# Performance work log

Measured on AMD Instinct MI355X. Metric: run time of the kernel, lower is better.

The kernel has to match this reference:

```python
import jax, jax.numpy as jnp
import numpy as np

B, T = 32, 512
DA, DV = 1280, 768
D = DA + DV          # fused audio+video feature dim = 2048
DM = 256             # mamba d_model
L = 4                # n_layers
DI = 2 * DM          # d_inner (expand=2)
DS = 16              # d_state
DC = 4               # d_conv
R = DM // 16         # dt_rank = ceil(256/16)
H = 128              # attn-pool hidden
NC = 8               # emotion classes
EPS_TIN = 1e-5
EPS_LN = 1e-5


def _ln(x, g, b):
    mu = x.mean(-1, keepdims=True)
    v = ((x - mu) ** 2).mean(-1, keepdims=True)
    return (x - mu) / jnp.sqrt(v + EPS_LN) * g + b


def _mamba(u, in_w, cw, cb, xw, dtw, dtb, A_log, Dp, ow):
    # u: [B,T,DM] -> [B,T,DM]; Mamba(v1) selective scan, d_state=16, d_conv=4, expand=2
    xz = jnp.einsum('btd,ed->bte', u, in_w)            # [B,T,2*DI]
    x, z = xz[..., :DI], xz[..., DI:]
    xp = jnp.pad(x, ((0, 0), (DC - 1, 0), (0, 0)))     # causal depthwise conv1d
    xc = sum(xp[:, k:k + u.shape[1], :] * cw[:, k] for k in range(DC)) + cb
    x = jax.nn.silu(xc)
    dbc = jnp.einsum('btd,ed->bte', x, xw)             # [B,T,R+2*DS]
    dt = jax.nn.softplus(jnp.einsum('btr,dr->btd', dbc[..., :R], dtw) + dtb)
    Bm = dbc[..., R:R + DS]
    Cm = dbc[..., R + DS:]
    A = -jnp.exp(A_log)                                # [DI,DS]

    def step(h, inp):
        dt_t, B_t, C_t, x_t = inp                      # [B,DI],[B,DS],[B,DS],[B,DI]
        h = jnp.exp(dt_t[..., None] * A) * h + dt_t[..., None] * B_t[:, None, :] * x_t[..., None]
        return h, jnp.einsum('bds,bs->bd', h, C_t)

    h0 = jnp.zeros((u.shape[0], DI, DS), u.dtype)
    xs = (dt.swapaxes(0, 1), Bm.swapaxes(0, 1), Cm.swapaxes(0, 1), x.swapaxes(0, 1))
    _, ys = jax.lax.scan(step, h0, xs)
    y = ys.swapaxes(0, 1) + Dp * x
    y = y * jax.nn.silu(z)
    return jnp.einsum('bti,oi->bto', y, ow)


def _forward(x, tin_gamma, tin_beta, proj_w, proj_b, ln_g, ln_b, in_proj_w, conv_w, conv_b,
             x_proj_w, dt_proj_w, dt_proj_b, A_log, D_param, out_proj_w,
             out_ln_g, out_ln_b, res_scale, attn_w1, attn_b1, attn_w2, head_w, head_b, lengths):
    mask = jnp.arange(T)[None, :] < lengths[:, None]   # [B,T]
    m = mask[..., None].astype(x.dtype)
    # FusedTIN: masked temporal instance norm + affine
    denom = jnp.maximum(lengths, 1).astype(x.dtype)[:, None, None]
    mean = (x * m).sum(1, keepdims=True) / denom
    var = (((x - mean) ** 2) * m).sum(1, keepdims=True) / denom
    xn = (x - mean) / jnp.sqrt(var + EPS_TIN) * m
    xn = (xn * tin_gamma + tin_beta) * m
    # MambaStack: proj_in + prenorm residual mamba blocks (dropout = eval identity)
    h = jnp.einsum('btd,md->btm', xn, proj_w) + proj_b
    for l in range(L):
        y = _mamba(_ln(h, ln_g[l], ln_b[l]), in_proj_w[l], conv_w[l], conv_b[l],
                   x_proj_w[l], dt_proj_w[l], dt_proj_b[l], A_log[l], D_param[l], out_proj_w[l])
        h = h + res_scale * y
    h = _ln(h, out_ln_g, out_ln_b)
    # MaskedAttnPool
    s = jnp.einsum('bth,oh->bto', jnp.tanh(jnp.einsum('btd,hd->bth', h, attn_w1) + attn_b1), attn_w2)[..., 0]
    logits = jnp.where(mask, s, -jnp.inf)
    alpha = jnp.nan_to_num(jax.nn.softmax(logits, axis=1)) * mask
    alpha = alpha / jnp.clip(alpha.sum(1, keepdims=True), 1e-9)
    ctx = (alpha[..., None] * h).sum(1)
    # classifier head
    return jnp.einsum('bd,cd->bc', ctx, head_w) + head_b


def setup_inputs() -> dict:
    key = jax.random.key(0)
    ks = jax.random.split(key, 16)
    s = 0.05
    inp = {}
    inp['x'] = jax.random.normal(ks[0], (B, T, D), jnp.float32)
    inp['lengths'] = jax.random.randint(ks[1], (B,), T // 4, T + 1)
    inp['tin_gamma'] = jnp.ones((D,), jnp.float32)
    inp['tin_beta'] = jnp.zeros((D,), jnp.float32)
    inp['proj_w'] = jax.random.normal(ks[2], (DM, D), jnp.float32) * s
    inp['proj_b'] = jnp.zeros((DM,), jnp.float32)
    inp['ln_g'] = jnp.ones((L, DM), jnp.float32)
    inp['ln_b'] = jnp.zeros((L, DM), jnp.float32)
    inp['in_proj_w'] = jax.random.normal(ks[3], (L, 2 * DI, DM), jnp.float32) * s
    inp['conv_w'] = jax.random.normal(ks[4], (L, DI, DC), jnp.float32) * s
    inp['conv_b'] = jnp.zeros((L, DI), jnp.float32)
    inp['x_proj_w'] = jax.random.normal(ks[5], (L, R + 2 * DS, DI), jnp.float32) * s
    inp['dt_proj_w'] = jax.random.normal(ks[6], (L, DI, R), jnp.float32) * s
    inp['dt_proj_b'] = jnp.full((L, DI), -3.0, jnp.float32) + jax.random.normal(ks[7], (L, DI), jnp.float32) * 0.1
    inp['A_log'] = jnp.log(jnp.broadcast_to(jnp.arange(1, DS + 1, dtype=jnp.float32), (L, DI, DS)) + 0.0)
    inp['D_param'] = jnp.ones((L, DI), jnp.float32)
    inp['out_proj_w'] = jax.random.normal(ks[8], (L, DM, DI), jnp.float32) * s
    inp['out_ln_g'] = jnp.ones((DM,), jnp.float32)
    inp['out_ln_b'] = jnp.zeros((DM,), jnp.float32)
    inp['res_scale'] = jnp.asarray(0.1, jnp.float32)
    inp['attn_w1'] = jax.random.normal(ks[9], (H, DM), jnp.float32) * s
    inp['attn_b1'] = jnp.zeros((H,), jnp.float32)
    inp['attn_w2'] = jax.random.normal(ks[10], (1, H), jnp.float32) * s
    inp['head_w'] = jax.random.normal(ks[11], (NC, DM), jnp.float32) * s
    inp['head_b'] = jnp.zeros((NC,), jnp.float32)
    return inp


def reference(x, tin_gamma, tin_beta, proj_w, proj_b, ln_g, ln_b, in_proj_w, conv_w, conv_b,
              x_proj_w, dt_proj_w, dt_proj_b, A_log, D_param, out_proj_w,
              out_ln_g, out_ln_b, res_scale, attn_w1, attn_b1, attn_w2, head_w, head_b, lengths):
    return _forward(x, tin_gamma, tin_beta, proj_w, proj_b, ln_g, ln_b, in_proj_w, conv_w, conv_b,
                    x_proj_w, dt_proj_w, dt_proj_b, A_log, D_param, out_proj_w,
                    out_ln_g, out_ln_b, res_scale, attn_w1, attn_b1, attn_w2, head_w, head_b, lengths)
```

## Files before the change

### kernel.cpp

```cpp
#include <hip/hip_runtime.h>

#define NB 32
#define NT 512
#define ND 2048
#define NDM 256
#define NDI 512
#define NDS 16
#define NR 16
#define NH 128
#define NNC 8
#define NL 4
#define NM (NB*NT)

typedef __attribute__((ext_vector_type(8))) short short8;
typedef __attribute__((ext_vector_type(4))) float floatx4;

__device__ __forceinline__ unsigned short f2bf_rn(float f) {
    unsigned u = __builtin_bit_cast(unsigned, f);
    u += 0x7FFFu + ((u >> 16) & 1u);
    return (unsigned short)(u >> 16);
}
__device__ __forceinline__ void cvt8(const float* v, short8& h8, short8& l8) {
#pragma unroll
    for (int q = 0; q < 8; ++q) {
        unsigned short hb = f2bf_rn(v[q]);
        float hf = __builtin_bit_cast(float, (unsigned)hb << 16);
        h8[q] = (short)hb;
        l8[q] = (short)f2bf_rn(v[q] - hf);
    }
}

__global__ __launch_bounds__(256) void tin_stats_k(
    const float* __restrict__ x, const int* __restrict__ lengths,
    float* __restrict__ mean, float* __restrict__ rstd)
{
    __shared__ float rs_[4][64];
    __shared__ float rq_[4][64];
    const int b = blockIdx.x >> 5;
    const int d0 = (blockIdx.x & 31) << 6;
    const int dl = threadIdx.x & 63;
    const int strip = threadIdx.x >> 6;
    const int len = lengths[b];
    const int d = d0 + dl;
    float s = 0.f, q = 0.f;
    for (int t = strip; t < len; t += 4) {
        float v = x[((size_t)(b*NT + t))*ND + d];
        s += v; q += v*v;
    }
    rs_[strip][dl] = s; rq_[strip][dl] = q;
    __syncthreads();
    if (threadIdx.x < 64) {
        float S = rs_[0][dl]+rs_[1][dl]+rs_[2][dl]+rs_[3][dl];
        float Q = rq_[0][dl]+rq_[1][dl]+rq_[2][dl]+rq_[3][dl];
        float inv = 1.f / (float)(len < 1 ? 1 : len);
        float mu = S * inv;
        float var = Q * inv - mu*mu;
        mean[b*ND + d] = mu;
        rstd[b*ND + d] = rsqrtf(var + 1e-5f);
    }
}

#define SLN 264
__global__ __launch_bounds__(256) void tin_norm_k(
    const float* __restrict__ x, const int* __restrict__ lengths,
    const float* __restrict__ mean, const float* __restrict__ rstd,
    const float* __restrict__ g, const float* __restrict__ be,
    short* __restrict__ Oh, short* __restrict__ Ol)
{
    __shared__ float sT[16][SLN];
    const int tid = threadIdx.x;
    const int row = tid >> 4, c = tid & 15;
    const int m = blockIdx.x*16 + row;
    const int b = m >> 9, t = m & (NT-1);
    const int len = lengths[b];
    const int kg0 = blockIdx.y*256 + c*16;
    if (t >= len) {
#pragma unroll
        for (int i = 0; i < 16; ++i) sT[row][c*16 + i] = 0.f;
    } else {
#pragma unroll
        for (int qq = 0; qq < 4; ++qq) {
            const int kg = kg0 + qq*4;
            float4 v = *(const float4*)(x + (size_t)m*ND + kg);
            float4 mn = *(const float4*)(mean + b*ND + kg);
            float4 rr = *(const float4*)(rstd + b*ND + kg);
            float4 gg = *(const float4*)(g + kg);
            float4 bb = *(const float4*)(be + kg);
            sT[row][c*16+qq*4+0] = (v.x-mn.x)*rr.x*gg.x + bb.x;
            sT[row][c*16+qq*4+1] = (v.y-mn.y)*rr.y*gg.y + bb.y;
            sT[row][c*16+qq*4+2] = (v.z-mn.z)*rr.z*gg.z + bb.z;
            sT[row][c*16+qq*4+3] = (v.w-mn.w)*rr.w*gg.w + bb.w;
        }
    }
    __syncthreads();
#pragma unroll
    for (int q = 0; q < 2; ++q) {
        const int slot = tid + 256*q;
        const int tile = slot >> 6, ln2 = slot & 63;
        const int mr = ln2 & 15, kc = ln2 >> 4;
        float v[8];
        *(float4*)&v[0] = *(const float4*)&sT[mr][tile*32 + kc*8];
        *(float4*)&v[4] = *(const float4*)&sT[mr][tile*32 + kc*8 + 4];
        short8 h8, l8; cvt8(v, h8, l8);
        const size_t off = ((size_t)blockIdx.x*64 + blockIdx.y*8 + tile)*512 + ln2*8;
        *(short8*)(Oh + off) = h8;
        *(short8*)(Ol + off) = l8;
    }
}

__global__ __launch_bounds__(256) void wconv_k(
    const float* __restrict__ W, short* __restrict__ Oh, short* __restrict__ Ol,
    int K, int nmod, int nvalid)
{
    __shared__ float sT[16][SLN];
    const int tid = threadIdx.x;
    const int row = tid >> 4, c = tid & 15;
    const int n = blockIdx.x*16 + row;
    const int rr = n % nmod;
    const int kg0 = blockIdx.y*256 + c*16;
    if (rr >= nvalid) {
#pragma unroll
        for (int i = 0; i < 16; ++i) sT[row][c*16 + i] = 0.f;
    } else {
        const int src = (n/nmod)*nvalid + rr;
#pragma unroll
        for (int qq = 0; qq < 4; ++qq) {
            float4 v = *(const float4*)(W + (size_t)src*K + kg0 + qq*4);
            *(float4*)&sT[row][c*16+qq*4] = v;
        }
    }
    __syncthreads();
#pragma unroll
    for (int q = 0; q < 2; ++q) {
        const int slot = tid + 256*q;
        const int tile = slot >> 6, ln2 = slot & 63;
        const int mr = ln2 & 15, kc = ln2 >> 4;
        float v[8];
        *(float4*)&v[0] = *(const float4*)&sT[mr][tile*32 + kc*8];
        *(float4*)&v[4] = *(const float4*)&sT[mr][tile*32 + kc*8 + 4];
        short8 h8, l8; cvt8(v, h8, l8);
        const size_t off = ((size_t)blockIdx.x*(K>>5) + blockIdx.y*8 + tile)*512 + ln2*8;
        *(short8*)(Oh + off) = h8;
        *(short8*)(Ol + off) = l8;
    }
}

template<int MSUB, int NSUB, int EPI>
__global__ __launch_bounds__(256) void mgemm_k(
    const short* __restrict__ Ah, const short* __restrict__ Al,
    const short* __restrict__ Bh, const short* __restrict__ Bl,
    const float* __restrict__ bias, float* __restrict__ C,
    int ldc, int Nvalid, int K, const float* __restrict__ rsp)
{
    __shared__ __align__(16) short lds[(MSUB+NSUB)*1024];
    short* As_h = lds;
    short* As_l = lds + MSUB*512;
    short* Bs_h = lds + MSUB*1024;
    short* Bs_l = lds + MSUB*1024 + NSUB*512;
    const int tid = threadIdx.x, lane = tid & 63, w = tid >> 6;
    const int m0t = blockIdx.x * MSUB;
    const int n0t = blockIdx.y * NSUB;
    const int Ktiles = K >> 5;
    constexpr int MI = MSUB/2, NI = NSUB/2;
    constexpr int ASG = MSUB/4, BSG = NSUB/4;
    const int wm = w >> 1, wn = w & 1;

    floatx4 acc[MI][NI] = {};
    short8 rah[ASG], ral[ASG], rbh[BSG], rbl[BSG];

#pragma unroll
    for (int u = 0; u < ASG; ++u) {
        const size_t off = ((size_t)(m0t + w*ASG + u)*Ktiles)*512 + lane*8;
        rah[u] = *(const short8*)(Ah + off); ral[u] = *(const short8*)(Al + off);
    }
#pragma unroll
    for (int u = 0; u < BSG; ++u) {
        const size_t off = ((size_t)(n0t + w*BSG + u)*Ktiles)*512 + lane*8;
        rbh[u] = *(const short8*)(Bh + off); rbl[u] = *(const short8*)(Bl + off);
    }

    for (int kb = 0; kb < Ktiles; ++kb) {
        __syncthreads();
#pragma unroll
        for (int u = 0; u < ASG; ++u) {
            const int sub = w*ASG + u;
            *(short8*)&As_h[sub*512 + lane*8] = rah[u];
            *(short8*)&As_l[sub*512 + lane*8] = ral[u];
        }
#pragma unroll
        for (int u = 0; u < BSG; ++u) {
            const int sub = w*BSG + u;
            *(short8*)&Bs_h[sub*512 + lane*8] = rbh[u];
            *(short8*)&Bs_l[sub*512 + lane*8] = rbl[u];
        }
        __syncthreads();
        if (kb + 1 < Ktiles) {
#pragma unroll
            for (int u = 0; u < ASG; ++u) {
                const size_t off = ((size_t)(m0t + w*ASG + u)*Ktiles + kb + 1)*512 + lane*8;
                rah[u] = *(const short8*)(Ah + off); ral[u] = *(const short8*)(Al + off);
            }
#pragma unroll
            for (int u = 0; u < BSG; ++u) {
                const size_t off = ((size_t)(n0t + w*BSG + u)*Ktiles + kb + 1)*512 + lane*8;
                rbh[u] = *(const short8*)(Bh + off); rbl[u] = *(const short8*)(Bl + off);
            }
        }
        short8 fah[MI], fal[MI], fbh[NI], fbl[NI];
#pragma unroll
        for (int i = 0; i < MI; ++i) {
            const int sub = wm*MI + i;
            fah[i] = *(const short8*)&As_h[sub*512 + lane*8];
            fal[i] = *(const short8*)&As_l[sub*512 + lane*8];
        }
#pragma unroll
        for (int j = 0; j < NI; ++j) {
            const int sub = wn*NI + j;
            fbh[j] = *(const short8*)&Bs_h[sub*512 + lane*8];
            fbl[j] = *(const short8*)&Bs_l[sub*512 + lane*8];
        }
#pragma unroll
        for (int i = 0; i < MI; ++i)
#pragma unroll
            for (int j = 0; j < NI; ++j) {
                acc[i][j] = __builtin_amdgcn_mfma_f32_16x16x32_bf16(fah[i], fbh[j], acc[i][j], 0, 0, 0);
                acc[i][j] = __builtin_amdgcn_mfma_f32_16x16x32_bf16(fah[i], fbl[j], acc[i][j], 0, 0, 0);
                acc[i][j] = __builtin_amdgcn_mfma_f32_16x16x32_bf16(fal[i], fbh[j], acc[i][j], 0, 0, 0);
            }
    }

    const float rs = (EPI == 1) ? rsp[0] : 0.f;
    const int lc = lane >> 4, col = lane & 15;
#pragma unroll
    for (int j = 0; j < NI; ++j) {
        const int n = (n0t + wn*NI + j)*16 + col;
        if (n < Nvalid) {
            const float bv = (EPI != 1 && bias) ? bias[n] : 0.f;
#pragma unroll
            for (int i = 0; i < MI; ++i) {
                const int mb = (m0t + wm*MI + i)*16 + lc*4;
#pragma unroll
                for (int r = 0; r < 4; ++r) {
                    float v = acc[i][j][r];
                    float* cp = C + (size_t)(mb + r)*ldc + n;
                    if (EPI == 0)      *cp = v + bv;
                    else if (EPI == 1) *cp = fmaf(rs, v, *cp);
                    else               *cp = tanhf(v + bv);
                }
            }
        }
    }
}

template<int WF32>
__global__ __launch_bounds__(256) void ln_blk_k(
    const float* __restrict__ in, const float* __restrict__ g,
    const float* __restrict__ b,
    short* __restrict__ Oh, short* __restrict__ Ol, float* __restrict__ o32)
{
    __shared__ float sT[16][SLN];
    const int tid = threadIdx.x;
    const int row = tid >> 4, c = tid & 15;
    const int m = blockIdx.x*16 + row;
    float v[16];
#pragma unroll
    for (int qq = 0; qq < 4; ++qq)
        *(float4*)&v[qq*4] = *(const float4*)(in + (size_t)m*NDM + c*16 + qq*4);
    float s = 0.f, q = 0.f;
#pragma unroll
    for (int i = 0; i < 16; ++i) { s += v[i]; q += v[i]*v[i]; }
#pragma unroll
    for (int o = 8; o; o >>= 1) { s += __shfl_xor(s, o); q += __shfl_xor(q, o); }
    const float mu = s * (1.f/NDM);
    const float r = rsqrtf(q*(1.f/NDM) - mu*mu + 1e-5f);
#pragma unroll
    for (int i = 0; i < 16; ++i) {
        const int kg = c*16 + i;
        v[i] = (v[i]-mu)*r*g[kg] + b[kg];
        sT[row][kg] = v[i];
    }
    if (WF32) {
#pragma unroll
        for (int qq = 0; qq < 4; ++qq)
            *(float4*)(o32 + (size_t)m*NDM + c*16 + qq*4) = *(const float4*)&v[qq*4];
    }
    __syncthreads();
#pragma unroll
    for (int qv = 0; qv < 2; ++qv) {
        const int slot = tid + 256*qv;
        const int tile = slot >> 6, ln2 = slot & 63;
        const int mr = ln2 & 15, kc = ln2 >> 4;
        float vv[8];
        *(float4*)&vv[0] = *(const float4*)&sT[mr][tile*32 + kc*8];
        *(float4*)&vv[4] = *(const float4*)&sT[mr][tile*32 + kc*8 + 4];
        short8 h8, l8; cvt8(vv, h8, l8);
        const size_t off = ((size_t)blockIdx.x*8 + tile)*512 + ln2*8;
        *(short8*)(Oh + off) = h8;
        *(short8*)(Ol + off) = l8;
    }
}

#define SCV 520
__global__ __launch_bounds__(256) void conv_blk_k(
    const float* __restrict__ xz, const float* __restrict__ cw,
    const float* __restrict__ cb, float* __restrict__ xc32,
    short* __restrict__ Oh, short* __restrict__ Ol)
{
    __shared__ float sT[16][SCV];
    const int tid = threadIdx.x;
    const int row = tid >> 4, cg = tid & 15;
    const int m = blockIdx.x*16 + row;
    const int t = m & (NT-1);
#pragma unroll
    for (int grp = 0; grp < 4; ++grp) {
        const int ch = cg*32 + grp*8;
        float a[8];
        *(float4*)&a[0] = *(const float4*)(cb + ch);
        *(float4*)&a[4] = *(const float4*)(cb + ch + 4);
        float4 wv[8];
#pragma unroll
        for (int i = 0; i < 8; ++i) wv[i] = *(const float4*)(cw + (ch+i)*4);
#pragma unroll
        for (int kk = 0; kk < 4; ++kk) {
            if (t - 3 + kk >= 0) {
                const float* xp = xz + (size_t)(m-3+kk)*(2*NDI) + ch;
                float xv[8];
                *(float4*)&xv[0] = *(const float4*)xp;
                *(float4*)&xv[4] = *(const float4*)(xp + 4);
                const float tap[8] = {
                    kk==0?wv[0].x:kk==1?wv[0].y:kk==2?wv[0].z:wv[0].w,
                    kk==0?wv[1].x:kk==1?wv[1].y:kk==2?wv[1].z:wv[1].w,
                    kk==0?wv[2].x:kk==1?wv[2].y:kk==2?wv[2].z:wv[2].w,
                    kk==0?wv[3].x:kk==1?wv[3].y:kk==2?wv[3].z:wv[3].w,
                    kk==0?wv[4].x:kk==1?wv[4].y:kk==2?wv[4].z:wv[4].w,
                    kk==0?wv[5].x:kk==1?wv[5].y:kk==2?wv[5].z:wv[5].w,
                    kk==0?wv[6].x:kk==1?wv[6].y:kk==2?wv[6].z:wv[6].w,
                    kk==0?wv[7].x:kk==1?wv[7].y:kk==2?wv[7].z:wv[7].w};
#pragma unroll
                for (int i = 0; i < 8; ++i) a[i] = fmaf(xv[i], tap[i], a[i]);
            }
        }
#pragma unroll
        for (int i = 0; i < 8; ++i) a[i] = a[i] / (1.f + __expf(-a[i]));
        *(float4*)&sT[row][ch] = *(const float4*)&a[0];
        *(float4*)&sT[row][ch+4] = *(const float4*)&a[4];
        *(float4*)(xc32 + (size_t)m*NDI + ch) = *(const float4*)&a[0];
        *(float4*)(xc32 + (size_t)m*NDI + ch + 4) = *(const float4*)&a[4];
    }
    __syncthreads();
#pragma unroll
    for (int q = 0; q < 4; ++q) {
        const int slot = tid + 256*q;
        const int tile = slot >> 6, ln2 = slot & 63;
        const int mr = ln2 & 15, kc = ln2 >> 4;
        float vv[8];
        *(float4*)&vv[0] = *(const float4*)&sT[mr][tile*32 + kc*8];
        *(float4*)&vv[4] = *(const float4*)&sT[mr][tile*32 + kc*8 + 4];
        short8 h8, l8; cvt8(vv, h8, l8);
        const size_t off = ((size_t)blockIdx.x*16 + tile)*512 + ln2*8;
        *(short8*)(Oh + off) = h8;
        *(short8*)(Ol + off) = l8;
    }
}

__global__ __launch_bounds__(256) void dt_k(
    const float* __restrict__ dbc, const float* __restrict__ dtw,
    const float* __restrict__ dtb, float* __restrict__ dt)
{
    const int m = blockIdx.x;
    const float* rsrc = dbc + (size_t)m*48;
    float rv[16];
#pragma unroll
    for (int i = 0; i < 16; ++i) rv[i] = rsrc[i];
#pragma unroll
    for (int hh = 0; hh < 2; ++hh) {
        const int d = hh*256 + threadIdx.x;
        const float* wr = dtw + d*16;
        float a = dtb[d];
#pragma unroll
        for (int i = 0; i < 16; ++i) a = fmaf(rv[i], wr[i], a);
        dt[(size_t)m*NDI + d] = (a > 20.f) ? a : log1pf(__expf(a));
    }
}

__global__ __launch_bounds__(256) void scan_k(
    const float* __restrict__ dbc, const float* __restrict__ dtp,
    const float* __restrict__ xcp, const float* __restrict__ xz,
    const float* __restrict__ Alog, const float* __restrict__ Dp,
    short* __restrict__ Yh, short* __restrict__ Yl)
{
    __shared__ float sBC[64][32];
    __shared__ float sY[64][68];
    const int tid = threadIdx.x;
    const int w = tid >> 6, lane = tid & 63;
    const int dl = lane >> 2, sg = lane & 3;
    const int b = blockIdx.x >> 3;
    const int d0 = (blockIdx.x & 7) << 6;
    const int dloc = w*16 + dl;
    const int d = d0 + dloc;
    float ar[4];
    {
        float4 al4 = *(const float4*)(Alog + d*NDS + sg*4);
        ar[0] = -__expf(al4.x); ar[1] = -__expf(al4.y);
        ar[2] = -__expf(al4.z); ar[3] = -__expf(al4.w);
    }
    const float Dpv = Dp[d];
    float hr[4] = {0.f, 0.f, 0.f, 0.f};
    const int mbase = b*NT;
    const int srow = tid >> 2, sq = (tid & 3) << 3;

    for (int c0 = 0; c0 < NT; c0 += 64) {
        {
            const float* dp_ = dbc + (size_t)(mbase + c0 + srow)*48 + 16 + sq;
            *(float4*)&sBC[srow][sq]   = *(const float4*)dp_;
            *(float4*)&sBC[srow][sq+4] = *(const float4*)(dp_ + 4);
        }
        __syncthreads();
        float pdt[2][4], px[2][4];
#pragma unroll
        for (int u = 0; u < 4; ++u) {
            const size_t mm = (size_t)(mbase + c0 + u);
            pdt[0][u] = dtp[mm*NDI + d];
            px[0][u]  = xcp[mm*NDI + d];
        }
#pragma unroll
        for (int tg = 0; tg < 16; ++tg) {
            const int cur = tg & 1, nxt = cur ^ 1;
            if (tg < 15) {
#pragma unroll
                for (int u = 0; u < 4; ++u) {
                    const size_t mm = (size_t)(mbase + c0 + (tg+1)*4 + u);
                    pdt[nxt][u] = dtp[mm*NDI + d];
                    px[nxt][u]  = xcp[mm*NDI + d];
                }
            }
#pragma unroll
            for (int u = 0; u < 4; ++u) {
                const int tloc = tg*4 + u;
                const float dtv = pdt[cur][u], xv = px[cur][u];
                const float4 Bv = *(const float4*)&sBC[tloc][sg*4];
                const float4 Cv = *(const float4*)&sBC[tloc][16 + sg*4];
                const float dbx = dtv * xv;
                float cp;
                {
                    float pa = __expf(dtv*ar[0]); hr[0] = fmaf(pa, hr[0], dbx*Bv.x); cp = hr[0]*Cv.x;
                    pa = __expf(dtv*ar[1]); hr[1] = fmaf(pa, hr[1], dbx*Bv.y); cp = fmaf(hr[1], Cv.y, cp);
                    pa = __expf(dtv*ar[2]); hr[2] = fmaf(pa, hr[2], dbx*Bv.z); cp = fmaf(hr[2], Cv.z, cp);
                    pa = __expf(dtv*ar[3]); hr[3] = fmaf(pa, hr[3], dbx*Bv.w); cp = fmaf(hr[3], Cv.w, cp);
                }
                cp += __shfl_xor(cp, 1);
                cp += __shfl_xor(cp, 2);
                if (sg == 0) sY[tloc][dloc] = fmaf(Dpv, xv, cp);
            }
        }
        __syncthreads();
#pragma unroll
        for (int q = 0; q < 2; ++q) {
            const int slot = tid + 256*q;
            const int tile = slot >> 6, ln2 = slot & 63;
            const int tm = tile >> 1, tk = tile & 1;
            const int mr = ln2 & 15, kc = ln2 >> 4;
            const int m = mbase + c0 + tm*16 + mr;
            const int kd = d0 + tk*32 + kc*8;
            float yv[8];
            *(float4*)&yv[0] = *(const float4*)&sY[tm*16 + mr][tk*32 + kc*8];
            *(float4*)&yv[4] = *(const float4*)&sY[tm*16 + mr][tk*32 + kc*8 + 4];
            float zv[8];
            *(float4*)&zv[0] = *(const float4*)(xz + (size_t)m*(2*NDI) + NDI + kd);
            *(float4*)&zv[4] = *(const float4*)(xz + (size_t)m*(2*NDI) + NDI + kd + 4);
#pragma unroll
            for (int i = 0; i < 8; ++i)
                yv[i] *= zv[i] / (1.f + __expf(-zv[i]));
            short8 h8, l8; cvt8(yv, h8, l8);
            const size_t off = ((size_t)(m>>4)*16 + (kd>>5))*512 + ln2*8;
            *(short8*)(Yh + off) = h8;
            *(short8*)(Yl + off) = l8;
        }
        __syncthreads();
    }
}

__global__ __launch_bounds__(64) void score_k(
    const float* __restrict__ t1, const float* __restrict__ w2,
    float* __restrict__ sout)
{
    const int m = blockIdx.x;
    const int lane = threadIdx.x;
    float v = t1[(size_t)m*NH + lane]*w2[lane]
            + t1[(size_t)m*NH + 64 + lane]*w2[64 + lane];
#pragma unroll
    for (int o = 32; o; o >>= 1) v += __shfl_xor(v, o);
    if (lane == 0) sout[m] = v;
}

__global__ __launch_bounds__(256) void pool_k(
    const float* __restrict__ sbuf, const float* __restrict__ u,
    const int* __restrict__ lengths, float* __restrict__ ctx)
{
    __shared__ float al[NT];
    __shared__ float red[256];
    const int b = blockIdx.x;
    const int tid = threadIdx.x;
    const int len = lengths[b];
    float mx = -3.4e38f;
    for (int t = tid; t < len; t += 256) mx = fmaxf(mx, sbuf[b*NT + t]);
    red[tid] = mx; __syncthreads();
    for (int o = 128; o; o >>= 1) { if (tid < o) red[tid] = fmaxf(red[tid], red[tid+o]); __syncthreads(); }
    mx = red[0];
    __syncthreads();
    float sm = 0.f;
    for (int t = tid; t < len; t += 256) {
        float e = __expf(sbuf[b*NT + t] - mx);
        al[t] = e; sm += e;
    }
    red[tid] = sm; __syncthreads();
    for (int o = 128; o; o >>= 1) { if (tid < o) red[tid] += red[tid+o]; __syncthreads(); }
    const float rZ = 1.f / red[0];
    float acc = 0.f;
    const float* up = u + (size_t)b*NT*NDM + tid;
    for (int t = 0; t < len; ++t) acc = fmaf(al[t], up[(size_t)t*NDM], acc);
    ctx[b*NDM + tid] = acc * rZ;
}

__global__ __launch_bounds__(64) void head_k(
    const float* __restrict__ ctx, const float* __restrict__ hw,
    const float* __restrict__ hb, float* __restrict__ o)
{
    const int b = blockIdx.x;
    const int lane = threadIdx.x;
    const float4 c4 = *(const float4*)(ctx + b*NDM + lane*4);
#pragma unroll
    for (int c = 0; c < NNC; ++c) {
        const float4 w4 = *(const float4*)(hw + c*NDM + lane*4);
        float v = c4.x*w4.x + c4.y*w4.y + c4.z*w4.z + c4.w*w4.w;
#pragma unroll
        for (int off = 32; off; off >>= 1) v += __shfl_xor(v, off);
        if (lane == 0) o[b*NNC + c] = v + hb[c];
    }
}

extern "C" void kernel_launch(void* const* d_in, const int* in_sizes, int n_in,
                              void* d_out, int out_size, void* d_ws, size_t ws_size,
                              hipStream_t stream)
{
    (void)in_sizes; (void)n_in; (void)out_size; (void)ws_size;
    const float* x         = (const float*)d_in[0];
    const int*   lengths   = (const int*)  d_in[1];
    const float* tin_gamma = (const float*)d_in[2];
    const float* tin_beta  = (const float*)d_in[3];
    const float* proj_w    = (const float*)d_in[4];
    const float* proj_b    = (const float*)d_in[5];
    const float* ln_g      = (const float*)d_in[6];
    const float* ln_b      = (const float*)d_in[7];
    const float* in_proj_w = (const float*)d_in[8];
    const float* conv_w    = (const float*)d_in[9];
    const float* conv_b    = (const float*)d_in[10];
    const float* x_proj_w  = (const float*)d_in[11];
    const float* dt_proj_w = (const float*)d_in[12];
    const float* dt_proj_b = (const float*)d_in[13];
    const float* A_log     = (const float*)d_in[14];
    const float* D_param   = (const float*)d_in[15];
    const float* out_proj_w= (const float*)d_in[16];
    const float* out_ln_g  = (const float*)d_in[17];
    const float* out_ln_b  = (const float*)d_in[18];
    const float* res_scale = (const float*)d_in[19];
    const float* attn_w1   = (const float*)d_in[20];
    const float* attn_b1   = (const float*)d_in[21];
    const float* attn_w2   = (const float*)d_in[22];
    const float* head_w    = (const float*)d_in[23];
    const float* head_b    = (const float*)d_in[24];
    float* out = (float*)d_out;

    float* ws = (float*)d_ws;
    float* mean   = ws;
    float* rstd   = mean + 65536;
    float* hbuf   = rstd + 65536;
    float* ubuf32 = hbuf + (size_t)NM*NDM;
    float* dbc    = ubuf32 + (size_t)NM*NDM;
    float* t1     = dbc + (size_t)NM*48;
    float* sbuf   = t1 + (size_t)NM*NH;
    float* ctx    = sbuf + NM;
    float* fend   = ctx + NB*NDM;
    short* ublk_h = (short*)fend;
    short* ublk_l = ublk_h + (size_t)NM*NDM;
    short* xcb_h  = ublk_l + (size_t)NM*NDM;
    short* xcb_l  = xcb_h + (size_t)NM*NDI;
    short* yq_h   = xcb_l + (size_t)NM*NDI;
    short* yq_l   = yq_h + (size_t)NM*NDI;
    short* pw_h   = yq_l + (size_t)NM*NDI;
    short* pw_l   = pw_h + (size_t)256*2048;
    short* iw_h   = pw_l + (size_t)256*2048;
    short* iw_l   = iw_h + (size_t)4*1024*256;
    short* xw_h   = iw_l + (size_t)4*1024*256;
    short* xw_l   = xw_h + (size_t)4*64*512;
    short* ow_h   = xw_l + (size_t)4*64*512;
    short* ow_l   = ow_h + (size_t)4*256*512;
    short* aw_h   = ow_l + (size_t)4*256*512;
    short* aw_l   = aw_h + (size_t)128*256;
    float* over   = (float*)(aw_l + (size_t)128*256);
    short* xn_h   = (short*)over;
    short* xn_l   = xn_h + (size_t)NM*ND;
    float* xz     = over;
    float* xc32   = over + (size_t)NM*2*NDI;
    float* dtb_   = xc32 + (size_t)NM*NDI;

    const dim3 blk(256);

    wconv_k<<<dim3(16, 8), blk, 0, stream>>>(proj_w, pw_h, pw_l, 2048, 1<<28, 1<<28);
    wconv_k<<<dim3(256, 1), blk, 0, stream>>>(in_proj_w, iw_h, iw_l, 256, 1<<28, 1<<28);
    wconv_k<<<dim3(16, 2), blk, 0, stream>>>(x_proj_w, xw_h, xw_l, 512, 64, 48);
    wconv_k<<<dim3(64, 2), blk, 0, stream>>>(out_proj_w, ow_h, ow_l, 512, 1<<28, 1<<28);
    wconv_k<<<dim3(8, 1), blk, 0, stream>>>(attn_w1, aw_h, aw_l, 256, 1<<28, 1<<28);

    tin_stats_k<<<dim3(NB*32), blk, 0, stream>>>(x, lengths, mean, rstd);
    tin_norm_k<<<dim3(NM/16, 8), blk, 0, stream>>>(x, lengths, mean, rstd,
        tin_gamma, tin_beta, xn_h, xn_l);
    mgemm_k<4,8,0><<<dim3(256, 2), blk, 0, stream>>>(
        xn_h, xn_l, pw_h, pw_l, proj_b, hbuf, NDM, NDM, 2048, nullptr);

    for (int l = 0; l < NL; ++l) {
        ln_blk_k<0><<<dim3(NM/16), blk, 0, stream>>>(
            hbuf, ln_g + l*NDM, ln_b + l*NDM, ublk_h, ublk_l, nullptr);
        mgemm_k<8,8,0><<<dim3(128, 8), blk, 0, stream>>>(
            ublk_h, ublk_l, iw_h + (size_t)l*1024*256, iw_l + (size_t)l*1024*256,
            nullptr, xz, 2*NDI, 2*NDI, NDM, nullptr);
        conv_blk_k<<<dim3(NM/16), blk, 0, stream>>>(
            xz, conv_w + (size_t)l*NDI*4, conv_b + (size_t)l*NDI, xc32, xcb_h, xcb_l);
        mgemm_k<4,4,0><<<dim3(256, 1), blk, 0, stream>>>(
            xcb_h, xcb_l, xw_h + (size_t)l*64*512, xw_l + (size_t)l*64*512,
            nullptr, dbc, 48, 48, 512, nullptr);
        dt_k<<<dim3(NM), blk, 0, stream>>>(
            dbc, dt_proj_w + (size_t)l*NDI*NR, dt_proj_b + (size_t)l*NDI, dtb_);
        scan_k<<<dim3(NB*8), blk, 0, stream>>>(
            dbc, dtb_, xc32, xz, A_log + (size_t)l*NDI*NDS, D_param + (size_t)l*NDI,
            yq_h, yq_l);
        mgemm_k<4,8,1><<<dim3(256, 2), blk, 0, stream>>>(
            yq_h, yq_l, ow_h + (size_t)l*256*512, ow_l + (size_t)l*256*512,
            nullptr, hbuf, NDM, NDM, 512, res_scale);
    }

    ln_blk_k<1><<<dim3(NM/16), blk, 0, stream>>>(
        hbuf, out_ln_g, out_ln_b, ublk_h, ublk_l, ubuf32);
    mgemm_k<4,8,2><<<dim3(256, 1), blk, 0, stream>>>(
        ublk_h, ublk_l, aw_h, aw_l, attn_b1, t1, NH, NH, 256, nullptr);
    score_k<<<dim3(NM), dim3(64), 0, stream>>>(t1, attn_w2, sbuf);
    pool_k<<<dim3(NB), blk, 0, stream>>>(sbuf, ubuf32, lengths, ctx);
    head_k<<<dim3(NB), dim3(64), 0, stream>>>(ctx, head_w, head_b, out);
}
```

Before: 1.644 ms.

## Stage dt and x chunks in shared memory and use DPP quad reductions in scan

The scan kernel now loads each 64-timestep chunk of dt and conv output with coalesced float4 global reads and stores it transposed into shared memory, replacing per-timestep scalar global loads with strided addresses. B/C and dt/x values are double-buffered from LDS in registers. The quad reduction uses DPP row-permute instructions instead of shuffles. The barrier moves to the top of the chunk loop. The cost is extra LDS space and bank conflicts on the transposed stores, which may lower occupancy.

```diff
diff --git a/kernel.cpp b/kernel.cpp
--- a/kernel.cpp
+++ b/kernel.cpp
@@ -28,6 +28,15 @@
         h8[q] = (short)hb;
         l8[q] = (short)f2bf_rn(v[q] - hf);
     }
+}
+__device__ __forceinline__ float quad_sum(float v) {
+    int i = __builtin_bit_cast(int, v);
+    int j = __builtin_amdgcn_update_dpp(0, i, 0xB1, 0xF, 0xF, true);
+    v += __builtin_bit_cast(float, j);
+    i = __builtin_bit_cast(int, v);
+    j = __builtin_amdgcn_update_dpp(0, i, 0x4E, 0xF, 0xF, true);
+    v += __builtin_bit_cast(float, j);
+    return v;
 }
 
 __global__ __launch_bounds__(256) void tin_stats_k(
@@ -390,6 +399,8 @@
     short* __restrict__ Yh, short* __restrict__ Yl)
 {
     __shared__ float sBC[64][32];
+    __shared__ float sDt[64][68];
+    __shared__ float sX[64][68];
     __shared__ float sY[64][68];
     const int tid = threadIdx.x;
     const int w = tid >> 6, lane = tid & 63;
@@ -408,49 +419,70 @@
     float hr[4] = {0.f, 0.f, 0.f, 0.f};
     const int mbase = b*NT;
     const int srow = tid >> 2, sq = (tid & 3) << 3;
+    const int tr = tid >> 2, qq = tid & 3;
 
     for (int c0 = 0; c0 < NT; c0 += 64) {
+        __syncthreads();
         {
             const float* dp_ = dbc + (size_t)(mbase + c0 + srow)*48 + 16 + sq;
             *(float4*)&sBC[srow][sq]   = *(const float4*)dp_;
             *(float4*)&sBC[srow][sq+4] = *(const float4*)(dp_ + 4);
         }
+        {
+            const float* dsrc = dtp + (size_t)(mbase + c0 + tr)*NDI + d0 + qq*16;
+            const float* xsrc = xcp + (size_t)(mbase + c0 + tr)*NDI + d0 + qq*16;
+#pragma unroll
+            for (int i = 0; i < 4; ++i) {
+                float4 dv = *(const float4*)(dsrc + i*4);
+                float4 xv = *(const float4*)(xsrc + i*4);
+                const int dd = qq*16 + i*4;
+                sDt[dd+0][tr]=dv.x; sDt[dd+1][tr]=dv.y; sDt[dd+2][tr]=dv.z; sDt[dd+3][tr]=dv.w;
+                sX[dd+0][tr]=xv.x;  sX[dd+1][tr]=xv.y;  sX[dd+2][tr]=xv.z;  sX[dd+3][tr]=xv.w;
+            }
+        }
         __syncthreads();
-        float pdt[2][4], px[2][4];
-#pragma unroll
-        for (int u = 0; u < 4; ++u) {
-            const size_t mm = (size_t)(mbase + c0 + u);
-            pdt[0][u] = dtp[mm*NDI + d];
-            px[0][u]  = xcp[mm*NDI + d];
-        }
-#pragma unroll
-        for (int tg = 0; tg < 16; ++tg) {
-            const int cur = tg & 1, nxt = cur ^ 1;
-            if (tg < 15) {
-#pragma unroll
-                for (int u = 0; u < 4; ++u) {
-                    const size_t mm = (size_t)(mbase + c0 + (tg+1)*4 + u);
-                    pdt[nxt][u] = dtp[mm*NDI + d];
-                    px[nxt][u]  = xcp[mm*NDI + d];
+        float4 Bt[2][4], Ct[2][4], dt4[2], x4[2];
+#pragma unroll
+        for (int i = 0; i < 4; ++i) {
+            Bt[0][i] = *(const float4*)&sBC[i][sg*4];
+            Ct[0][i] = *(const float4*)&sBC[i][16 + sg*4];
+        }
+        dt4[0] = *(const float4*)&sDt[dloc][0];
+        x4[0]  = *(const float4*)&sX[dloc][0];
+#pragma unroll
+        for (int g = 0; g < 16; ++g) {
+            const int cur = g & 1, nxt = cur ^ 1;
+            if (g < 15) {
+                const int t4 = (g+1)*4;
+#pragma unroll
+                for (int i = 0; i < 4; ++i) {
+                    Bt[nxt][i] = *(const float4*)&sBC[t4+i][sg*4];
+                    Ct[nxt][i] = *(const float4*)&sBC[t4+i][16 + sg*4];
                 }
-            }
-#pragma unroll
-            for (int u = 0; u < 4; ++u) {
-                const int tloc = tg*4 + u;
-                const float dtv = pdt[cur][u], xv = px[cur][u];
-                const float4 Bv = *(const float4*)&sBC[tloc][sg*4];
-                const float4 Cv = *(const float4*)&sBC[tloc][16 + sg*4];
+                dt4[nxt] = *(const float4*)&sDt[dloc][t4];
+                x4[nxt]  = *(const float4*)&sX[dloc][t4];
+            }
+#pragma unroll
+            for (int i = 0; i < 4; ++i) {
+                const float dtv = (i==0)?dt4[cur].x:(i==1)?dt4[cur].y:(i==2)?dt4[cur].z:dt4[cur].w;
+                const float xv  = (i==0)?x4[cur].x:(i==1)?x4[cur].y:(i==2)?x4[cur].z:x4[cur].w;
+                const float4 Bv = Bt[cur][i];
+                const float4 Cv = Ct[cur][i];
                 const float dbx = dtv * xv;
-                float cp;
-                {
-                    float pa = __expf(dtv*ar[0]); hr[0] = fmaf(pa, hr[0], dbx*Bv.x); cp = hr[0]*Cv.x;
-                    pa = __expf(dtv*ar[1]); hr[1] = fmaf(pa, hr[1], dbx*Bv.y); cp = fmaf(hr[1], Cv.y, cp);
-                    pa = __expf(dtv*ar[2]); hr[2] = fmaf(pa, hr[2], dbx*Bv.z); cp = fmaf(hr[2], Cv.z, cp);
-                    pa = __expf(dtv*ar[3]); hr[3] = fmaf(pa, hr[3], dbx*Bv.w); cp = fmaf(hr[3], Cv.w, cp);
-                }
-                cp += __shfl_xor(cp, 1);
-                cp += __shfl_xor(cp, 2);
-                if (sg == 0) sY[tloc][dloc] = fmaf(Dpv, xv, cp);
+                float pa0 = __expf(dtv*ar[0]);
+                float pa1 = __expf(dtv*ar[1]);
+                float pa2 = __expf(dtv*ar[2]);
+                float pa3 = __expf(dtv*ar[3]);
+                hr[0] = fmaf(pa0, hr[0], dbx*Bv.x);
+                hr[1] = fmaf(pa1, hr[1], dbx*Bv.y);
+                hr[2] = fmaf(pa2, hr[2], dbx*Bv.z);
+                hr[3] = fmaf(pa3, hr[3], dbx*Bv.w);
+                float cp = hr[0]*Cv.x;
+                cp = fmaf(hr[1], Cv.y, cp);
+                cp = fmaf(hr[2], Cv.z, cp);
+                cp = fmaf(hr[3], Cv.w, cp);
+                cp = quad_sum(cp);
+                if (sg == 0) sY[g*4 + i][dloc] = fmaf(Dpv, xv, cp);
             }
         }
         __syncthreads();
@@ -476,7 +508,6 @@
             *(short8*)(Yh + off) = h8;
             *(short8*)(Yl + off) = l8;
         }
-        __syncthreads();
     }
 }
 
```

Result: faster. 1.501 ms (-8.7%).
